# Kernel tuning notes

Measured on AMD Instinct MI355X. Metric: run time of the kernel, lower is better.

The kernel has to match this reference:

```python
import jax, jax.numpy as jnp
import numpy as np

N = 50000      # nodes
E = 400000     # edges (before self-loops)
D_IN = 128     # input node features
H1, C1 = 8, 64   # layer-1 heads / per-head channels (concat -> 512)
H2, C2 = 1, 16   # layer-2 heads / per-head channels (mean -> 16)
NEG_SLOPE = 0.2  # PyG GATConv default leaky-relu slope


def setup_inputs() -> dict:
    key = jax.random.key(0)
    ks = jax.random.split(key, 10)
    x = jax.random.normal(ks[0], (N, D_IN), jnp.float32)
    edge_index = jax.random.randint(ks[1], (2, E), 0, N, dtype=jnp.int32)
    s1 = D_IN ** -0.5
    s2 = (H1 * C1) ** -0.5
    return {
        "x": x,
        "edge_index": edge_index,
        "W1": jax.random.normal(ks[2], (D_IN, H1 * C1), jnp.float32) * s1,
        "a1_src": jax.random.normal(ks[3], (H1, C1), jnp.float32) * (C1 ** -0.5),
        "a1_dst": jax.random.normal(ks[4], (H1, C1), jnp.float32) * (C1 ** -0.5),
        "b1": jnp.zeros((H1 * C1,), jnp.float32),
        "W2": jax.random.normal(ks[5], (H1 * C1, H2 * C2), jnp.float32) * s2,
        "a2_src": jax.random.normal(ks[6], (H2, C2), jnp.float32) * (C2 ** -0.5),
        "a2_dst": jax.random.normal(ks[7], (H2, C2), jnp.float32) * (C2 ** -0.5),
        "b2": jnp.zeros((C2,), jnp.float32),
    }


def gat_layer(x, W, a_src, a_dst, bias, src, dst, H, C, concat):
    n = x.shape[0]
    h = (x @ W).reshape(n, H, C)                       # [N,H,C]
    # per-node attention halves (PyG: alpha = a_src . h_src + a_dst . h_dst)
    al_src = jnp.einsum('nhc,hc->nh', h, a_src)        # [N,H]
    al_dst = jnp.einsum('nhc,hc->nh', h, a_dst)
    logits = jax.nn.leaky_relu(al_src[src] + al_dst[dst], NEG_SLOPE)  # [E,H]
    # segment softmax over incoming edges of each destination node
    m = jax.ops.segment_max(logits, dst, num_segments=n)
    e = jnp.exp(logits - m[dst])
    denom = jax.ops.segment_sum(e, dst, num_segments=n)
    alpha = e / denom[dst]                             # [E,H]
    out = jax.ops.segment_sum(alpha[:, :, None] * h[src], dst, num_segments=n)  # [N,H,C]
    out = out.reshape(n, H * C) if concat else out.mean(axis=1)
    return out + bias


def reference(x, edge_index, W1, a1_src, a1_dst, b1, W2, a2_src, a2_dst, b2):
    n = x.shape[0]
    # PyG GATConv adds self-loops by default (applied in each layer)
    loops = jnp.arange(n, dtype=edge_index.dtype)
    src = jnp.concatenate([edge_index[0], loops])
    dst = jnp.concatenate([edge_index[1], loops])
    h1 = gat_layer(x, W1, a1_src, a1_dst, b1, src, dst, H1, C1, True)   # [N,512]
    h1 = jax.nn.elu(h1)
    return gat_layer(h1, W2, a2_src, a2_dst, b2, src, dst, H2, C2, False)  # [N,16]
```

## Files before the change

### kernel.cpp

```cpp
#include <hip/hip_runtime.h>
#include <math.h>

#define N_NODES 50000
#define N_EDGES 400000
#define N_TOT   450000
#define NEG 0.2f
#define CAP 64

typedef __attribute__((ext_vector_type(8))) short bf16x8;
typedef __attribute__((ext_vector_type(8))) unsigned short u16x8;
typedef __attribute__((ext_vector_type(4))) float f32x4;

__device__ __forceinline__ float lrelu(float x) { return x > 0.f ? x : NEG * x; }

__device__ __forceinline__ unsigned short f2bf(float f) {
    unsigned u = __float_as_uint(f);
    unsigned r = u + 0x7FFFu + ((u >> 16) & 1u);
    return (unsigned short)(r >> 16);
}
__device__ __forceinline__ float bf2f(unsigned short h) {
    return __uint_as_float(((unsigned)h) << 16);
}

__global__ void k_init(const float* __restrict__ W1, unsigned short* W1hiT,
                       const float* __restrict__ W2, unsigned short* W2hiT,
                       const float* __restrict__ a1s, const float* __restrict__ a1d,
                       unsigned short* W1aThi, unsigned short* W1aTlo,
                       int* cursor) {
    int i = blockIdx.x * 256 + threadIdx.x;
    if (i < 128 * 512) {
        int col = i & 511, k = i >> 9;
        W1hiT[col * 128 + k] = f2bf(W1[k * 512 + col]);
    } else if (i < 128 * 512 + 512 * 16) {
        int j = i - 128 * 512;
        int col = j & 15, k = j >> 4;
        W2hiT[col * 512 + k] = f2bf(W2[k * 16 + col]);
    } else if (i < 128 * 512 + 512 * 16 + 128 * 16) {
        int j = i - (128 * 512 + 512 * 16);
        int c16 = j & 15, k = j >> 4;
        int hd = c16 & 7;
        const float* av = (c16 < 8) ? a1s : a1d;
        float acc = 0.f;
#pragma unroll 8
        for (int c = 0; c < 64; c++)
            acc = fmaf(W1[k * 512 + hd * 64 + c], av[hd * 64 + c], acc);
        unsigned short h = f2bf(acc);
        W1aThi[c16 * 128 + k] = h;
        W1aTlo[c16 * 128 + k] = f2bf(acc - bf2f(h));
    } else {
        int j = i - (128 * 512 + 512 * 16 + 128 * 16);
        if (j < N_NODES) cursor[j] = 0;
    }
}

#define SCAT 256
__global__ __launch_bounds__(256) void k_sg1(const int* __restrict__ ei,
                                             int* __restrict__ cursor,
                                             int* __restrict__ colsrc,
                                             const float* __restrict__ x,
                                             const unsigned short* __restrict__ W1hiT,
                                             const unsigned short* __restrict__ W1aThi,
                                             const unsigned short* __restrict__ W1aTlo,
                                             unsigned short* __restrict__ h1b,
                                             float* __restrict__ al1s,
                                             float* __restrict__ al1d) {
    __shared__ unsigned short xs_hi[64 * 136];
    if (blockIdx.x < SCAT) {
        int gtid = blockIdx.x * 256 + threadIdx.x;
        for (int i = gtid; i < N_TOT; i += SCAT * 256) {
            int src, dst;
            if (i < N_EDGES) { src = ei[i]; dst = ei[N_EDGES + i]; }
            else             { src = dst = i - N_EDGES; }
            int pos = atomicAdd(&cursor[dst], 1);
            if (pos < CAP) colsrc[dst * CAP + pos] = src;
        }
        return;
    }
    const int t = threadIdx.x;
    const int rb = (blockIdx.x - SCAT) * 64;

#pragma unroll
    for (int i = 0; i < 8; i++) {
        int idx = t + 256 * i;
        int r = idx >> 5;
        int k = (idx & 31) * 4;
        int gr = rb + r;
        float4 v = make_float4(0.f, 0.f, 0.f, 0.f);
        if (gr < N_NODES) v = *reinterpret_cast<const float4*>(&x[gr * 128 + k]);
        ushort4 hi;
        hi.x = f2bf(v.x); hi.y = f2bf(v.y); hi.z = f2bf(v.z); hi.w = f2bf(v.w);
        *reinterpret_cast<ushort4*>(&xs_hi[r * 136 + k]) = hi;
    }
    __syncthreads();

    const int lane = t & 63;
    const int w = t >> 6;
    const int kbase = (lane >> 4) * 8;
    const int colloc = (w << 4) + (lane & 15);

#pragma unroll
    for (int pr = 0; pr < 4; pr++) {
        bf16x8 bhi[2][4];
#pragma unroll
        for (int si = 0; si < 2; si++) {
            int col = (pr * 2 + si) * 64 + colloc;
#pragma unroll
            for (int kc = 0; kc < 4; kc++)
                bhi[si][kc] = *reinterpret_cast<const bf16x8*>(&W1hiT[col * 128 + kc * 32 + kbase]);
        }
#pragma unroll
        for (int mt = 0; mt < 4; mt++) {
            const int arow = mt * 16 + (lane & 15);
            bf16x8 ah[4];
#pragma unroll
            for (int kc = 0; kc < 4; kc++)
                ah[kc] = *reinterpret_cast<const bf16x8*>(&xs_hi[arow * 136 + kc * 32 + kbase]);
#pragma unroll
            for (int si = 0; si < 2; si++) {
                f32x4 acc = {0.f, 0.f, 0.f, 0.f};
#pragma unroll
                for (int kc = 0; kc < 4; kc++)
                    acc = __builtin_amdgcn_mfma_f32_16x16x32_bf16(ah[kc], bhi[si][kc], acc, 0, 0, 0);
                const int col = (pr * 2 + si) * 64 + colloc;
                const int r0 = rb + mt * 16 + (lane >> 4) * 4;
#pragma unroll
                for (int r = 0; r < 4; r++) {
                    int row = r0 + r;
                    if (row < N_NODES) h1b[row * 512 + col] = f2bf(acc[r]);
                }
            }
        }
    }

    {
        const int c16 = lane & 15;
        bf16x8 bh[4], bl[4];
#pragma unroll
        for (int kc = 0; kc < 4; kc++) {
            bh[kc] = *reinterpret_cast<const bf16x8*>(&W1aThi[c16 * 128 + kc * 32 + kbase]);
            bl[kc] = *reinterpret_cast<const bf16x8*>(&W1aTlo[c16 * 128 + kc * 32 + kbase]);
        }
        const int arow = (w << 4) + (lane & 15);
        f32x4 acc = {0.f, 0.f, 0.f, 0.f};
#pragma unroll
        for (int kc = 0; kc < 4; kc++) {
            bf16x8 ah = *reinterpret_cast<const bf16x8*>(&xs_hi[arow * 136 + kc * 32 + kbase]);
            acc = __builtin_amdgcn_mfma_f32_16x16x32_bf16(ah, bh[kc], acc, 0, 0, 0);
            acc = __builtin_amdgcn_mfma_f32_16x16x32_bf16(ah, bl[kc], acc, 0, 0, 0);
        }
        const int r0 = rb + (w << 4) + (lane >> 4) * 4;
#pragma unroll
        for (int r = 0; r < 4; r++) {
            int row = r0 + r;
            if (row < N_NODES) {
                if (c16 < 8) al1s[row * 8 + c16] = acc[r];
                else         al1d[row * 8 + (c16 - 8)] = acc[r];
            }
        }
    }
}

__global__ __launch_bounds__(512) void k_agg1(const int* __restrict__ cursor,
                                              const int* __restrict__ colsrc,
                                              const float* __restrict__ al1s,
                                              const float* __restrict__ al1d,
                                              const unsigned short* __restrict__ h1b,
                                              const float* __restrict__ b1,
                                              const unsigned short* __restrict__ W2hiT,
                                              const float* __restrict__ a2s,
                                              const float* __restrict__ a2d,
                                              unsigned short* __restrict__ h2b,
                                              float* __restrict__ al2s,
                                              float* __restrict__ al2d) {
    __shared__ float pw[4][8 * 66];
    __shared__ __align__(16) unsigned short vs[4 * 520];
    const int wv   = threadIdx.x >> 6;
    const int lane = threadIdx.x & 63;
    const int nd   = wv >> 1;
    const int half = wv & 1;
    const int n0 = blockIdx.x * 4;
    const int n  = n0 + nd;
    const int cnt = min(cursor[n], CAP);
    const int eb = n * CAP;
    const int h  = half * 4 + (lane >> 4);
    const int c4 = half * 256 + lane * 4;
    float* mypw = pw[nd];

    const float4 dh = *reinterpret_cast<const float4*>(&al1d[n * 8 + half * 4]);

    int s0 = 0;
    float p0 = 0.f, p1 = 0.f, p2 = 0.f, p3 = 0.f;
    if (lane < cnt) {
        s0 = colsrc[eb + lane];
        const float4 u = *reinterpret_cast<const float4*>(&al1s[s0 * 8 + half * 4]);
        p0 = __expf(fminf(lrelu(u.x + dh.x), 60.f));
        p1 = __expf(fminf(lrelu(u.y + dh.y), 60.f));
        p2 = __expf(fminf(lrelu(u.z + dh.z), 60.f));
        p3 = __expf(fminf(lrelu(u.w + dh.w), 60.f));
    }
    mypw[(half * 4 + 0) * 66 + lane] = p0;
    mypw[(half * 4 + 1) * 66 + lane] = p1;
    mypw[(half * 4 + 2) * 66 + lane] = p2;
    mypw[(half * 4 + 3) * 66 + lane] = p3;

    float acc0 = 0.f, acc1 = 0.f, acc2 = 0.f, acc3 = 0.f, sm = 0.f;
    const int pwh = h * 66;
    const int cnt8 = (cnt + 7) & ~7;

    for (int j = 0; j < cnt8; j += 8) {
        int s[8]; float w[8]; ushort4 vv[8];
#pragma unroll
        for (int k = 0; k < 8; k++) {
            s[k] = __shfl(s0, j + k, 64);
            w[k] = mypw[pwh + j + k];
        }
#pragma unroll
        for (int k = 0; k < 8; k++)
            vv[k] = *reinterpret_cast<const ushort4*>(&h1b[s[k] * 512 + c4]);
#pragma unroll
        for (int k = 0; k < 8; k++) {
            sm += w[k];
            acc0 = fmaf(w[k], bf2f(vv[k].x), acc0);
            acc1 = fmaf(w[k], bf2f(vv[k].y), acc1);
            acc2 = fmaf(w[k], bf2f(vv[k].z), acc2);
            acc3 = fmaf(w[k], bf2f(vv[k].w), acc3);
        }
    }

    const float inv = 1.f / sm;
    const float4 bb = *reinterpret_cast<const float4*>(&b1[c4]);
    float v0 = acc0 * inv + bb.x;
    float v1 = acc1 * inv + bb.y;
    float v2 = acc2 * inv + bb.z;
    float v3 = acc3 * inv + bb.w;
    v0 = v0 > 0.f ? v0 : __expf(v0) - 1.f;
    v1 = v1 > 0.f ? v1 : __expf(v1) - 1.f;
    v2 = v2 > 0.f ? v2 : __expf(v2) - 1.f;
    v3 = v3 > 0.f ? v3 : __expf(v3) - 1.f;
    ushort4 o;
    o.x = f2bf(v0); o.y = f2bf(v1); o.z = f2bf(v2); o.w = f2bf(v3);
    *reinterpret_cast<ushort4*>(&vs[nd * 520 + c4]) = o;

    __syncthreads();

    if (wv == 0) {
        const int col   = lane & 15;
        const int kbase = (lane >> 4) << 3;
        const int rowm  = lane & 3;
        f32x4 a2 = {0.f, 0.f, 0.f, 0.f};
#pragma unroll 4
        for (int kc = 0; kc < 16; kc++) {
            bf16x8 bh = *reinterpret_cast<const bf16x8*>(&W2hiT[col * 512 + kc * 32 + kbase]);
            bf16x8 ah = *reinterpret_cast<const bf16x8*>(&vs[rowm * 520 + kc * 32 + kbase]);
            a2 = __builtin_amdgcn_mfma_f32_16x16x32_bf16(ah, bh, a2, 0, 0, 0);
        }
        if (lane < 16) {
            const float as_c = a2s[col];
            const float ad_c = a2d[col];
#pragma unroll
            for (int r = 0; r < 4; r++) {
                float ps = a2[r] * as_c;
                float pd = a2[r] * ad_c;
                ps += __shfl_xor(ps, 1, 64); pd += __shfl_xor(pd, 1, 64);
                ps += __shfl_xor(ps, 2, 64); pd += __shfl_xor(pd, 2, 64);
                ps += __shfl_xor(ps, 4, 64); pd += __shfl_xor(pd, 4, 64);
                ps += __shfl_xor(ps, 8, 64); pd += __shfl_xor(pd, 8, 64);
                h2b[(n0 + r) * 16 + col] = f2bf(a2[r]);
                if (lane == 0) { al2s[n0 + r] = ps; al2d[n0 + r] = pd; }
            }
        }
    }
}

__global__ __launch_bounds__(256) void k_agg2(const int* __restrict__ cursor,
                                              const int* __restrict__ colsrc,
                                              const float* __restrict__ al2s,
                                              const float* __restrict__ al2d,
                                              const unsigned short* __restrict__ h2b,
                                              const float* __restrict__ b2,
                                              float* __restrict__ out) {
    int wv = threadIdx.x >> 6, lane = threadIdx.x & 63;
    int n = blockIdx.x * 4 + wv;
    if (n >= N_NODES) return;
    int cnt = min(cursor[n], CAP);
    const int eb = n * CAP;
    float ald = al2d[n];
    int q = lane >> 3;
    int c2 = (lane & 7) << 1;
    float acc0 = 0.f, acc1 = 0.f, smL = 0.f;
    for (int e = q; e < cnt; e += 8) {
        int s = colsrc[eb + e];
        float w = __expf(fminf(lrelu(al2s[s] + ald), 60.f));
        unsigned v = *reinterpret_cast<const unsigned*>(&h2b[s * 16 + c2]);
        smL += w;
        acc0 = fmaf(w, bf2f((unsigned short)(v & 0xFFFFu)), acc0);
        acc1 = fmaf(w, __uint_as_float(v & 0xFFFF0000u), acc1);
    }
    acc0 += __shfl_xor(acc0, 8, 64);  acc1 += __shfl_xor(acc1, 8, 64);  smL += __shfl_xor(smL, 8, 64);
    acc0 += __shfl_xor(acc0, 16, 64); acc1 += __shfl_xor(acc1, 16, 64); smL += __shfl_xor(smL, 16, 64);
    acc0 += __shfl_xor(acc0, 32, 64); acc1 += __shfl_xor(acc1, 32, 64); smL += __shfl_xor(smL, 32, 64);
    if (q == 0) {
        float inv = 1.f / smL;
        float2 r;
        r.x = acc0 * inv + b2[c2];
        r.y = acc1 * inv + b2[c2 + 1];
        *reinterpret_cast<float2*>(&out[n * 16 + c2]) = r;
    }
}

extern "C" void kernel_launch(void* const* d_in, const int* in_sizes, int n_in,
                              void* d_out, int out_size, void* d_ws, size_t ws_size,
                              hipStream_t stream) {
    const float* x   = (const float*)d_in[0];
    const int*   ei  = (const int*)d_in[1];
    const float* W1  = (const float*)d_in[2];
    const float* a1s = (const float*)d_in[3];
    const float* a1d = (const float*)d_in[4];
    const float* b1  = (const float*)d_in[5];
    const float* W2  = (const float*)d_in[6];
    const float* a2s = (const float*)d_in[7];
    const float* a2d = (const float*)d_in[8];
    const float* b2  = (const float*)d_in[9];
    float* out = (float*)d_out;

    char* ws = (char*)d_ws;
    unsigned short* h1b = (unsigned short*)(ws + 0);
    unsigned short* h2b = (unsigned short*)(ws + 102400000);
    float* al1s = (float*)(ws + 105600000);
    float* al1d = (float*)(ws + 107200000);
    float* al2s = (float*)(ws + 108800000);
    float* al2d = (float*)(ws + 109000000);
    int* cursor = (int*)(ws + 109200000);
    int* colsrc = (int*)(ws + 109400000);
    unsigned short* W1hiT  = (unsigned short*)(ws + 122200000);
    unsigned short* W2hiT  = (unsigned short*)(ws + 122336000);
    unsigned short* W1aThi = (unsigned short*)(ws + 122352384);
    unsigned short* W1aTlo = (unsigned short*)(ws + 122356480);

    k_init<<<492, 256, 0, stream>>>(W1, W1hiT, W2, W2hiT, a1s, a1d, W1aThi, W1aTlo, cursor);

    k_sg1<<<SCAT + (N_NODES + 63) / 64, 256, 0, stream>>>(ei, cursor, colsrc, x,
                                                          W1hiT, W1aThi, W1aTlo,
                                                          h1b, al1s, al1d);

    k_agg1<<<(N_NODES + 3) / 4, 512, 0, stream>>>(cursor, colsrc, al1s, al1d, h1b, b1,
                                                  W2hiT, a2s, a2d, h2b, al2s, al2d);

    k_agg2<<<(N_NODES + 3) / 4, 256, 0, stream>>>(cursor, colsrc, al2s, al2d, h2b, b2, out);
}
```

Measured before the change: 230.5 us.

## Restructure layer-1 aggregation: one wave per two nodes with prefetched 16B gathers

Each wave in the layer-1 aggregation kernel now handles two destination nodes across all 8 heads, and each lane gathers 8 bf16 channels (16 bytes) instead of 4. The edge loop is software-pipelined: the next two source rows are loaded while the current two are being consumed, and the two nodes' loops are interleaved to keep more independent loads in flight. Blocks shrink to 256 threads covering 8 nodes, and the fused layer-2 MFMA projection now fills 8 rows of the 16-row tile. The cost is higher register pressure from two sets of 8-wide accumulators and the prefetch buffers, which may lower occupancy.

After: 219.6 us. -4.7%, faster.

```diff
diff --git a/kernel.cpp b/kernel.cpp
--- a/kernel.cpp
+++ b/kernel.cpp
@@ -160,7 +160,21 @@
     }
 }
 
-__global__ __launch_bounds__(512) void k_agg1(const int* __restrict__ cursor,
+#define LDX(dst, s0reg, jj)                                                   \
+    { int s_ = __shfl(s0reg, (jj), 64);                                       \
+      dst = *reinterpret_cast<const u16x8*>(&h1b[s_ * 512 + c8]); }
+#define CONSA(buf, jj)                                                        \
+    { float w_ = pwA[pwh + (jj)]; smA += w_;                                  \
+      _Pragma("unroll")                                                       \
+      for (int c_ = 0; c_ < 8; c_++)                                          \
+          accA[c_] = fmaf(w_, bf2f(buf[c_]), accA[c_]); }
+#define CONSB(buf, jj)                                                        \
+    { float w_ = pwB[pwh + (jj)]; smB += w_;                                  \
+      _Pragma("unroll")                                                       \
+      for (int c_ = 0; c_ < 8; c_++)                                          \
+          accB[c_] = fmaf(w_, bf2f(buf[c_]), accB[c_]); }
+
+__global__ __launch_bounds__(256) void k_agg1(const int* __restrict__ cursor,
                                               const int* __restrict__ colsrc,
                                               const float* __restrict__ al1s,
                                               const float* __restrict__ al1d,
@@ -172,81 +186,120 @@
                                               unsigned short* __restrict__ h2b,
                                               float* __restrict__ al2s,
                                               float* __restrict__ al2d) {
-    __shared__ float pw[4][8 * 66];
-    __shared__ __align__(16) unsigned short vs[4 * 520];
+    __shared__ float pw[8][528];
+    __shared__ __align__(16) unsigned short vs[8 * 520];
     const int wv   = threadIdx.x >> 6;
     const int lane = threadIdx.x & 63;
-    const int nd   = wv >> 1;
-    const int half = wv & 1;
-    const int n0 = blockIdx.x * 4;
-    const int n  = n0 + nd;
-    const int cnt = min(cursor[n], CAP);
-    const int eb = n * CAP;
-    const int h  = half * 4 + (lane >> 4);
-    const int c4 = half * 256 + lane * 4;
-    float* mypw = pw[nd];
-
-    const float4 dh = *reinterpret_cast<const float4*>(&al1d[n * 8 + half * 4]);
-
-    int s0 = 0;
-    float p0 = 0.f, p1 = 0.f, p2 = 0.f, p3 = 0.f;
-    if (lane < cnt) {
-        s0 = colsrc[eb + lane];
-        const float4 u = *reinterpret_cast<const float4*>(&al1s[s0 * 8 + half * 4]);
-        p0 = __expf(fminf(lrelu(u.x + dh.x), 60.f));
-        p1 = __expf(fminf(lrelu(u.y + dh.y), 60.f));
-        p2 = __expf(fminf(lrelu(u.z + dh.z), 60.f));
-        p3 = __expf(fminf(lrelu(u.w + dh.w), 60.f));
-    }
-    mypw[(half * 4 + 0) * 66 + lane] = p0;
-    mypw[(half * 4 + 1) * 66 + lane] = p1;
-    mypw[(half * 4 + 2) * 66 + lane] = p2;
-    mypw[(half * 4 + 3) * 66 + lane] = p3;
-
-    float acc0 = 0.f, acc1 = 0.f, acc2 = 0.f, acc3 = 0.f, sm = 0.f;
+    const int n0 = blockIdx.x * 8;
+    const int nA = n0 + wv * 2;
+    const int nB = nA + 1;
+    const int cntA = min(cursor[nA], CAP);
+    const int cntB = min(cursor[nB], CAP);
+    const int h  = lane >> 3;
+    const int c8 = lane << 3;
     const int pwh = h * 66;
-    const int cnt8 = (cnt + 7) & ~7;
-
-    for (int j = 0; j < cnt8; j += 8) {
-        int s[8]; float w[8]; ushort4 vv[8];
+    float* pwA = pw[wv * 2];
+    float* pwB = pw[wv * 2 + 1];
+
+    int sA = 0, sB = 0;
+    if (lane < cntA) sA = colsrc[nA * CAP + lane];
+    if (lane < cntB) sB = colsrc[nB * CAP + lane];
+
+    u16x8 eA0, eA1, eB0, eB1;
+    LDX(eA0, sA, 0); LDX(eA1, sA, 1);
+    LDX(eB0, sB, 0); LDX(eB1, sB, 1);
+
+    {
+        const float4 dA0 = *reinterpret_cast<const float4*>(&al1d[nA * 8]);
+        const float4 dA1 = *reinterpret_cast<const float4*>(&al1d[nA * 8 + 4]);
+        const float4 dB0 = *reinterpret_cast<const float4*>(&al1d[nB * 8]);
+        const float4 dB1 = *reinterpret_cast<const float4*>(&al1d[nB * 8 + 4]);
+        float pA[8], pB[8];
+#pragma unroll
+        for (int k = 0; k < 8; k++) { pA[k] = 0.f; pB[k] = 0.f; }
+        if (lane < cntA) {
+            const float4 u0 = *reinterpret_cast<const float4*>(&al1s[sA * 8]);
+            const float4 u1 = *reinterpret_cast<const float4*>(&al1s[sA * 8 + 4]);
+            pA[0] = __expf(fminf(lrelu(u0.x + dA0.x), 60.f));
+            pA[1] = __expf(fminf(lrelu(u0.y + dA0.y), 60.f));
+            pA[2] = __expf(fminf(lrelu(u0.z + dA0.z), 60.f));
+            pA[3] = __expf(fminf(lrelu(u0.w + dA0.w), 60.f));
+            pA[4] = __expf(fminf(lrelu(u1.x + dA1.x), 60.f));
+            pA[5] = __expf(fminf(lrelu(u1.y + dA1.y), 60.f));
+            pA[6] = __expf(fminf(lrelu(u1.z + dA1.z), 60.f));
+            pA[7] = __expf(fminf(lrelu(u1.w + dA1.w), 60.f));
+        }
+        if (lane < cntB) {
+            const float4 u0 = *reinterpret_cast<const float4*>(&al1s[sB * 8]);
+            const float4 u1 = *reinterpret_cast<const float4*>(&al1s[sB * 8 + 4]);
+            pB[0] = __expf(fminf(lrelu(u0.x + dB0.x), 60.f));
+            pB[1] = __expf(fminf(lrelu(u0.y + dB0.y), 60.f));
+            pB[2] = __expf(fminf(lrelu(u0.z + dB0.z), 60.f));
+            pB[3] = __expf(fminf(lrelu(u0.w + dB0.w), 60.f));
+            pB[4] = __expf(fminf(lrelu(u1.x + dB1.x), 60.f));
+            pB[5] = __expf(fminf(lrelu(u1.y + dB1.y), 60.f));
+            pB[6] = __expf(fminf(lrelu(u1.z + dB1.z), 60.f));
+            pB[7] = __expf(fminf(lrelu(u1.w + dB1.w), 60.f));
+        }
 #pragma unroll
         for (int k = 0; k < 8; k++) {
-            s[k] = __shfl(s0, j + k, 64);
-            w[k] = mypw[pwh + j + k];
-        }
-#pragma unroll
-        for (int k = 0; k < 8; k++)
-            vv[k] = *reinterpret_cast<const ushort4*>(&h1b[s[k] * 512 + c4]);
+            pwA[k * 66 + lane] = pA[k];
+            pwB[k * 66 + lane] = pB[k];
+        }
+    }
+
+    float accA[8] = {0.f, 0.f, 0.f, 0.f, 0.f, 0.f, 0.f, 0.f};
+    float accB[8] = {0.f, 0.f, 0.f, 0.f, 0.f, 0.f, 0.f, 0.f};
+    float smA = 0.f, smB = 0.f;
+    const int mA = (cntA + 1) & ~1;
+    const int mB = (cntB + 1) & ~1;
+
+    int j = 0;
+    while (true) {
+        u16x8 tA0, tA1, tB0, tB1;
+        const bool cA = (j + 2) < mA;
+        const bool cB = (j + 2) < mB;
+        if (cA) { LDX(tA0, sA, j + 2); LDX(tA1, sA, j + 3); }
+        if (cB) { LDX(tB0, sB, j + 2); LDX(tB1, sB, j + 3); }
+        if (j < mA) { CONSA(eA0, j); CONSA(eA1, j + 1); }
+        if (j < mB) { CONSB(eB0, j); CONSB(eB1, j + 1); }
+        if (!cA && !cB) break;
+        eA0 = tA0; eA1 = tA1; eB0 = tB0; eB1 = tB1;
+        j += 2;
+    }
+
+    {
+        const float4 ba = *reinterpret_cast<const float4*>(&b1[c8]);
+        const float4 bb = *reinterpret_cast<const float4*>(&b1[c8 + 4]);
+        const float invA = 1.f / smA;
+        const float invB = 1.f / smB;
+        float vA[8], vB[8];
+        vA[0] = accA[0] * invA + ba.x; vA[1] = accA[1] * invA + ba.y;
+        vA[2] = accA[2] * invA + ba.z; vA[3] = accA[3] * invA + ba.w;
+        vA[4] = accA[4] * invA + bb.x; vA[5] = accA[5] * invA + bb.y;
+        vA[6] = accA[6] * invA + bb.z; vA[7] = accA[7] * invA + bb.w;
+        vB[0] = accB[0] * invB + ba.x; vB[1] = accB[1] * invB + ba.y;
+        vB[2] = accB[2] * invB + ba.z; vB[3] = accB[3] * invB + ba.w;
+        vB[4] = accB[4] * invB + bb.x; vB[5] = accB[5] * invB + bb.y;
+        vB[6] = accB[6] * invB + bb.z; vB[7] = accB[7] * invB + bb.w;
 #pragma unroll
         for (int k = 0; k < 8; k++) {
-            sm += w[k];
-            acc0 = fmaf(w[k], bf2f(vv[k].x), acc0);
-            acc1 = fmaf(w[k], bf2f(vv[k].y), acc1);
-            acc2 = fmaf(w[k], bf2f(vv[k].z), acc2);
-            acc3 = fmaf(w[k], bf2f(vv[k].w), acc3);
-        }
-    }
-
-    const float inv = 1.f / sm;
-    const float4 bb = *reinterpret_cast<const float4*>(&b1[c4]);
-    float v0 = acc0 * inv + bb.x;
-    float v1 = acc1 * inv + bb.y;
-    float v2 = acc2 * inv + bb.z;
-    float v3 = acc3 * inv + bb.w;
-    v0 = v0 > 0.f ? v0 : __expf(v0) - 1.f;
-    v1 = v1 > 0.f ? v1 : __expf(v1) - 1.f;
-    v2 = v2 > 0.f ? v2 : __expf(v2) - 1.f;
-    v3 = v3 > 0.f ? v3 : __expf(v3) - 1.f;
-    ushort4 o;
-    o.x = f2bf(v0); o.y = f2bf(v1); o.z = f2bf(v2); o.w = f2bf(v3);
-    *reinterpret_cast<ushort4*>(&vs[nd * 520 + c4]) = o;
+            vA[k] = vA[k] > 0.f ? vA[k] : __expf(vA[k]) - 1.f;
+            vB[k] = vB[k] > 0.f ? vB[k] : __expf(vB[k]) - 1.f;
+        }
+        u16x8 oA, oB;
+#pragma unroll
+        for (int k = 0; k < 8; k++) { oA[k] = f2bf(vA[k]); oB[k] = f2bf(vB[k]); }
+        *reinterpret_cast<u16x8*>(&vs[(wv * 2) * 520 + c8]) = oA;
+        *reinterpret_cast<u16x8*>(&vs[(wv * 2 + 1) * 520 + c8]) = oB;
+    }
 
     __syncthreads();
 
     if (wv == 0) {
         const int col   = lane & 15;
         const int kbase = (lane >> 4) << 3;
-        const int rowm  = lane & 3;
+        const int rowm  = lane & 7;
         f32x4 a2 = {0.f, 0.f, 0.f, 0.f};
 #pragma unroll 4
         for (int kc = 0; kc < 16; kc++) {
@@ -254,9 +307,10 @@
             bf16x8 ah = *reinterpret_cast<const bf16x8*>(&vs[rowm * 520 + kc * 32 + kbase]);
             a2 = __builtin_amdgcn_mfma_f32_16x16x32_bf16(ah, bh, a2, 0, 0, 0);
         }
-        if (lane < 16) {
+        if (lane < 32) {
             const float as_c = a2s[col];
             const float ad_c = a2d[col];
+            const int rbase = n0 + (lane >> 4) * 4;
 #pragma unroll
             for (int r = 0; r < 4; r++) {
                 float ps = a2[r] * as_c;
@@ -265,8 +319,8 @@
                 ps += __shfl_xor(ps, 2, 64); pd += __shfl_xor(pd, 2, 64);
                 ps += __shfl_xor(ps, 4, 64); pd += __shfl_xor(pd, 4, 64);
                 ps += __shfl_xor(ps, 8, 64); pd += __shfl_xor(pd, 8, 64);
-                h2b[(n0 + r) * 16 + col] = f2bf(a2[r]);
-                if (lane == 0) { al2s[n0 + r] = ps; al2d[n0 + r] = pd; }
+                h2b[(rbase + r) * 16 + col] = f2bf(a2[r]);
+                if ((lane & 15) == 0) { al2s[rbase + r] = ps; al2d[rbase + r] = pd; }
             }
         }
     }
@@ -343,8 +397,8 @@
                                                           W1hiT, W1aThi, W1aTlo,
                                                           h1b, al1s, al1d);
 
-    k_agg1<<<(N_NODES + 3) / 4, 512, 0, stream>>>(cursor, colsrc, al1s, al1d, h1b, b1,
-                                                  W2hiT, a2s, a2d, h2b, al2s, al2d);
+    k_agg1<<<N_NODES / 8, 256, 0, stream>>>(cursor, colsrc, al1s, al1d, h1b, b1,
+                                            W2hiT, a2s, a2d, h2b, al2s, al2d);
 
     k_agg2<<<(N_NODES + 3) / 4, 256, 0, stream>>>(cursor, colsrc, al2s, al2d, h2b, b2, out);
 }
```
